# Kernel optimization log

Hardware: AMD Instinct MI355X
Metric: run time of the kernel (lower is better)

Reference implementation:

```python
import jax, jax.numpy as jnp
import numpy as np


def setup_inputs() -> dict:
    key = jax.random.key(0)
    ks = jax.random.split(key, 6)
    B, C, H, W = 8, 128, 64, 64
    return {
        "curr_features": jax.random.normal(ks[0], (B, C, H, W), jnp.float32),
        "w1": jax.random.normal(ks[1], (C, 2 * C), jnp.float32) * 0.05,   # conv1x1 (2C->C)
        "b1": jnp.zeros((C,), jnp.float32),
        "gamma": jnp.ones((C,), jnp.float32),
        "beta": jnp.zeros((C,), jnp.float32),
        "running_mean": jax.random.normal(ks[2], (C,), jnp.float32) * 0.1,
        "running_var": jax.random.uniform(ks[3], (C,), jnp.float32, 0.5, 1.5),
        "w2": jax.random.normal(ks[4], (1, C), jnp.float32) * 0.05,       # conv1x1 (C->1)
        "b2": jnp.zeros((1,), jnp.float32),
    }


def reference(curr_features, w1, b1, gamma, beta, running_mean, running_var, w2, b2):
    B, C, H, W = curr_features.shape
    M = H * W
    BN_EPS = 1e-5
    LEAKY_SLOPE = 0.01  # InPlaceABNSync default activation: leaky_relu(0.01)

    f = curr_features.reshape(B, C, M)                       # [B,C,M]
    scores = jnp.einsum('bcm,bcn->bmn', f, f) * (C ** -0.5)  # [B,M,M]
    p = jax.nn.softmax(scores, axis=-1)
    feats1 = jnp.einsum('bmn,bcn->bcm', p, f)                # [B,C,M]

    x = jnp.concatenate([feats1, f], axis=1).reshape(B, 2 * C, H, W)

    # cls head: conv1x1 -> BN(inference) -> leaky_relu -> (dropout=identity in eval) -> conv1x1
    y = jnp.einsum('oc,bchw->bohw', w1, x) + b1[None, :, None, None]
    scale = gamma / jnp.sqrt(running_var + BN_EPS)
    y = (y - running_mean[None, :, None, None]) * scale[None, :, None, None] + beta[None, :, None, None]
    y = jnp.where(y >= 0, y, LEAKY_SLOPE * y)
    pred = jnp.einsum('oc,bchw->bohw', w2, y) + b2[None, :, None, None]  # [B,1,H,W]
    return pred
```

## Files before the change

### kernel.cpp

```cpp
#include <hip/hip_runtime.h>

#define NB 8
#define NC 128
#define NM 4096
#define FRAG 512

typedef __attribute__((ext_vector_type(8))) short short8;
typedef __attribute__((ext_vector_type(4))) float floatx4;

#define MFMA(a, b, c) __builtin_amdgcn_mfma_f32_16x16x32_bf16(a, b, c, 0, 0, 0)
#define EXP2F(x) __builtin_amdgcn_exp2f(x)

union S8U { short8 v; uint2 u2[2]; };

__device__ __forceinline__ unsigned pack2bf(float a, float b) {
    unsigned ua = __float_as_uint(a);
    unsigned ub = __float_as_uint(b);
    ua += 0x7fffu + ((ua >> 16) & 1u);
    ub += 0x7fffu + ((ub >> 16) & 1u);
    return (ua >> 16) | (ub & 0xffff0000u);
}

__constant__ float SF_C = 0.35712442f;
__constant__ float RS_C = 2.8001530f;


__global__ __launch_bounds__(256) void k_prep_f(
    const float* __restrict__ f, unsigned short* __restrict__ fX)
{
    __shared__ float Ls[128][65];
    const int tid = threadIdx.x;
    const int b   = blockIdx.x & 7;
    const int m0  = (blockIdx.x >> 3) * 64;
    const float* fb = f + (size_t)b * NC * NM;
    #pragma unroll
    for (int k = 0; k < 32; ++k) {
        int idx = tid + k * 256;
        int c = idx >> 6, mm = idx & 63;
        Ls[c][mm] = fb[(size_t)c * NM + m0 + mm];
    }
    __syncthreads();
    const float sf = SF_C;
    const int m  = tid >> 2;
    const int ks = tid & 3;
    const int ch = ks * 32;
    unsigned pk[16];
    #pragma unroll
    for (int i = 0; i < 16; ++i)
        pk[i] = pack2bf(Ls[ch + 2 * i][m] * sf, Ls[ch + 2 * i + 1][m] * sf);
    const int Mg  = m0 + m;
    const int mt  = Mg >> 4;
    const int lmm = Mg & 15;
    unsigned short* dst = fX + ((size_t)b * 256 + mt) * 4 * FRAG + ks * FRAG;
    #pragma unroll
    for (int q = 0; q < 4; ++q)
        *(uint4*)(dst + (q * 16 + lmm) * 8) =
            make_uint4(pk[4 * q], pk[4 * q + 1], pk[4 * q + 2], pk[4 * q + 3]);
}

__global__ __launch_bounds__(256) void k_prep_g(
    const unsigned short* __restrict__ fX, const float* __restrict__ w1,
    unsigned short* __restrict__ gX)
{
    __shared__ unsigned short gt[128][136];
    const int tid = threadIdx.x;
    const int wv  = tid >> 6;
    const int l   = tid & 63;
    const int lm  = l & 15;
    const int lq  = l >> 4;
    const int b    = blockIdx.x & 7;
    const int nblk = blockIdx.x >> 3;

    const float rs = RS_C;

    short8 wf2[2][4];
    #pragma unroll
    for (int j = 0; j < 2; ++j) {
        const int o = (wv * 2 + j) * 16 + lm;
        #pragma unroll
        for (int ks = 0; ks < 4; ++ks) {
            const float* wp = w1 + (size_t)o * (2 * NC) + ks * 32 + lq * 8;
            S8U t;
            t.u2[0] = make_uint2(pack2bf(wp[0] * rs, wp[1] * rs),
                                 pack2bf(wp[2] * rs, wp[3] * rs));
            t.u2[1] = make_uint2(pack2bf(wp[4] * rs, wp[5] * rs),
                                 pack2bf(wp[6] * rs, wp[7] * rs));
            wf2[j][ks] = t.v;
        }
    }

    const unsigned short* fXb = fX + (size_t)b * NM * NC;
    #pragma unroll 2
    for (int nt = 0; nt < 8; ++nt) {
        short8 af[4];
        #pragma unroll
        for (int ks = 0; ks < 4; ++ks)
            af[ks] = *(const short8*)
                (fXb + (size_t)(nblk * 8 + nt) * 4 * FRAG + ks * FRAG + l * 8);
        #pragma unroll
        for (int j = 0; j < 2; ++j) {
            floatx4 D = {0.f, 0.f, 0.f, 0.f};
            #pragma unroll
            for (int ks = 0; ks < 4; ++ks)
                D = MFMA(af[ks], wf2[j][ks], D);
            *(uint2*)&gt[(wv * 2 + j) * 16 + lm][nt * 16 + lq * 4] =
                make_uint2(pack2bf(D[0], D[1]), pack2bf(D[2], D[3]));
        }
    }
    __syncthreads();

    #pragma unroll
    for (int j = 0; j < 2; ++j) {
        const int ot = wv * 2 + j;
        #pragma unroll
        for (int k2 = 0; k2 < 4; ++k2) {
            uint4 v = *(const uint4*)&gt[ot * 16 + lm][k2 * 32 + lq * 8];
            *(uint4*)(gX + (((size_t)b * 32 + nblk) * 8 + ot) * 4 * FRAG
                      + k2 * FRAG + l * 8) = v;
        }
    }
}

__global__ __launch_bounds__(256, 2) void k_attn(
    const unsigned short* __restrict__ fX,
    const unsigned short* __restrict__ gX,
    const float* __restrict__ w1,
    const float* __restrict__ b1v, const float* __restrict__ gammav,
    const float* __restrict__ betav, const float* __restrict__ rmeanv,
    const float* __restrict__ rvarv, const float* __restrict__ w2v,
    const float* __restrict__ b2v, float* __restrict__ out)
{
    __shared__ unsigned short Ps[2][64][136];
    __shared__ float lpart[4][64];
    __shared__ float opart[4][64];

    const int tid = threadIdx.x;
    const int w   = tid >> 6;
    const int l   = tid & 63;
    const int lm  = l & 15;
    const int lq  = l >> 4;
    const int b   = blockIdx.x & 7;
    const int m0  = (blockIdx.x >> 3) * 64;

    const unsigned short* fXb = fX + (size_t)b * NM * NC;
    const unsigned short* gXb = gX + (size_t)b * NC * NM;

    short8 qf[4][4];
    {
        const int qt0 = m0 >> 4;
        #pragma unroll
        for (int mt = 0; mt < 4; ++mt)
            #pragma unroll
            for (int ks = 0; ks < 4; ++ks)
                qf[mt][ks] = *(const short8*)
                    (fXb + (size_t)(qt0 + mt) * 4 * FRAG + ks * FRAG + l * 8);
    }

    const unsigned short* kpA = fXb + (size_t)w * 4 * FRAG + l * 8;
    const unsigned short* kpB = fXb + (size_t)(4 + w) * 4 * FRAG + l * 8;
    const unsigned short* gp0 = gXb + (size_t)(2 * w) * 4 * FRAG + l * 8;
    const unsigned short* gp1 = gXb + (size_t)(2 * w + 1) * 4 * FRAG + l * 8;

    short8 kfA[4], kfB[4], gf0[4], gf1[4];
    #pragma unroll
    for (int ks = 0; ks < 4; ++ks) {
        kfA[ks] = *(const short8*)(kpA + ks * FRAG);
        kfB[ks] = *(const short8*)(kpB + ks * FRAG);
    }
    #pragma unroll
    for (int k2 = 0; k2 < 4; ++k2) {
        gf0[k2] = *(const short8*)(gp0 + k2 * FRAG);
        gf1[k2] = *(const short8*)(gp1 + k2 * FRAG);
    }

    floatx4 u[4][2];
    float lsum[4] = {0.f, 0.f, 0.f, 0.f};
    #pragma unroll
    for (int mt = 0; mt < 4; ++mt) {
        u[mt][0] = (floatx4){0.f, 0.f, 0.f, 0.f};
        u[mt][1] = (floatx4){0.f, 0.f, 0.f, 0.f};
    }

    for (int it = 0; it < 32; ++it) {
        const int buf = it & 1;

        floatx4 svA[4], svB[4];
        #pragma unroll
        for (int mt = 0; mt < 4; ++mt) {
            floatx4 a = {-24.f, -24.f, -24.f, -24.f};
            floatx4 bb = {-24.f, -24.f, -24.f, -24.f};
            #pragma unroll
            for (int ks = 0; ks < 4; ++ks) {
                a  = MFMA(kfA[ks], qf[mt][ks], a);
                bb = MFMA(kfB[ks], qf[mt][ks], bb);
            }
            svA[mt] = a; svB[mt] = bb;
        }
        {
            const int kstep = (it < 31) ? 8 * 4 * FRAG : 0;
            kpA += kstep; kpB += kstep;
            #pragma unroll
            for (int ks = 0; ks < 4; ++ks) {
                kfA[ks] = *(const short8*)(kpA + ks * FRAG);
                kfB[ks] = *(const short8*)(kpB + ks * FRAG);
            }
        }

        #pragma unroll
        for (int mt = 0; mt < 4; ++mt) {
            float pA0 = EXP2F(svA[mt][0]);
            float pA1 = EXP2F(svA[mt][1]);
            float pA2 = EXP2F(svA[mt][2]);
            float pA3 = EXP2F(svA[mt][3]);
            float pB0 = EXP2F(svB[mt][0]);
            float pB1 = EXP2F(svB[mt][1]);
            float pB2 = EXP2F(svB[mt][2]);
            float pB3 = EXP2F(svB[mt][3]);
            lsum[mt] += ((pA0 + pA1) + (pA2 + pA3)) +
                        ((pB0 + pB1) + (pB2 + pB3));
            *(uint2*)&Ps[buf][mt * 16 + lm][w * 16 + lq * 4] =
                make_uint2(pack2bf(pA0, pA1), pack2bf(pA2, pA3));
            *(uint2*)&Ps[buf][mt * 16 + lm][64 + w * 16 + lq * 4] =
                make_uint2(pack2bf(pB0, pB1), pack2bf(pB2, pB3));
        }
        __syncthreads();

        #pragma unroll
        for (int k2 = 0; k2 < 4; ++k2) {
            short8 pf[4];
            #pragma unroll
            for (int mt = 0; mt < 4; ++mt)
                pf[mt] = *(const short8*)&Ps[buf][mt * 16 + lm][k2 * 32 + lq * 8];
            #pragma unroll
            for (int mt = 0; mt < 4; ++mt) {
                u[mt][0] = MFMA(pf[mt], gf0[k2], u[mt][0]);
                u[mt][1] = MFMA(pf[mt], gf1[k2], u[mt][1]);
            }
        }
        {
            const int gstep = (it < 31) ? 8 * 4 * FRAG : 0;
            gp0 += gstep; gp1 += gstep;
            #pragma unroll
            for (int k2 = 0; k2 < 4; ++k2) {
                gf0[k2] = *(const short8*)(gp0 + k2 * FRAG);
                gf1[k2] = *(const short8*)(gp1 + k2 * FRAG);
            }
        }
    }

    #pragma unroll
    for (int mt = 0; mt < 4; ++mt) {
        lsum[mt] += __shfl_xor(lsum[mt], 16);
        lsum[mt] += __shfl_xor(lsum[mt], 32);
    }
    if (lq == 0) {
        #pragma unroll
        for (int mt = 0; mt < 4; ++mt)
            lpart[w][mt * 16 + lm] = lsum[mt];
    }

    floatx4 hacc[4][2];
    {
        const float rs = RS_C;
        #pragma unroll
        for (int j = 0; j < 2; ++j) {
            int o = w * 32 + j * 16 + lm;
            short8 wf[4];
            #pragma unroll
            for (int ks = 0; ks < 4; ++ks) {
                const float* wp = w1 + (size_t)o * (2 * NC) + NC + ks * 32 + lq * 8;
                S8U t;
                t.u2[0] = make_uint2(pack2bf(wp[0] * rs, wp[1] * rs),
                                     pack2bf(wp[2] * rs, wp[3] * rs));
                t.u2[1] = make_uint2(pack2bf(wp[4] * rs, wp[5] * rs),
                                     pack2bf(wp[6] * rs, wp[7] * rs));
                wf[ks] = t.v;
            }
            #pragma unroll
            for (int mt = 0; mt < 4; ++mt) {
                floatx4 a = {0.f, 0.f, 0.f, 0.f};
                #pragma unroll
                for (int ks = 0; ks < 4; ++ks)
                    a = MFMA(qf[mt][ks], wf[ks], a);
                hacc[mt][j] = a;
            }
        }
    }
    __syncthreads();

    float Abn[2], Dbn[2], W2[2];
    #pragma unroll
    for (int j = 0; j < 2; ++j) {
        int o = w * 32 + j * 16 + lm;
        float Ar = gammav[o] * rsqrtf(rvarv[o] + 1e-5f);
        Abn[j] = Ar;
        Dbn[j] = (b1v[o] - rmeanv[o]) * Ar + betav[o];
        W2[j]  = w2v[o];
    }
    float av[16];
    #pragma unroll
    for (int mt = 0; mt < 4; ++mt) {
        float4 L0 = *(const float4*)&lpart[0][mt * 16 + lq * 4];
        float4 L1 = *(const float4*)&lpart[1][mt * 16 + lq * 4];
        float4 L2 = *(const float4*)&lpart[2][mt * 16 + lq * 4];
        float4 L3 = *(const float4*)&lpart[3][mt * 16 + lq * 4];
        float4 Lt;
        Lt.x = (L0.x + L1.x) + (L2.x + L3.x);
        Lt.y = (L0.y + L1.y) + (L2.y + L3.y);
        Lt.z = (L0.z + L1.z) + (L2.z + L3.z);
        Lt.w = (L0.w + L1.w) + (L2.w + L3.w);
        #pragma unroll
        for (int r = 0; r < 4; ++r) {
            float rl = 1.f / ((const float*)&Lt)[r];
            float t0 = Abn[0] * (u[mt][0][r] * rl + hacc[mt][0][r]) + Dbn[0];
            float t1 = Abn[1] * (u[mt][1][r] * rl + hacc[mt][1][r]) + Dbn[1];
            t0 = t0 >= 0.f ? t0 : 0.01f * t0;
            t1 = t1 >= 0.f ? t1 : 0.01f * t1;
            av[mt * 4 + r] = W2[0] * t0 + W2[1] * t1;
        }
    }
    #pragma unroll
    for (int i = 0; i < 16; ++i) {
        av[i] += __shfl_xor(av[i], 1);
        av[i] += __shfl_xor(av[i], 2);
        av[i] += __shfl_xor(av[i], 4);
        av[i] += __shfl_xor(av[i], 8);
    }
    if (lm == 0) {
        #pragma unroll
        for (int mt = 0; mt < 4; ++mt)
            #pragma unroll
            for (int r = 0; r < 4; ++r)
                opart[w][mt * 16 + lq * 4 + r] = av[mt * 4 + r];
    }
    __syncthreads();
    if (tid < 64)
        out[(size_t)b * NM + m0 + tid] =
            b2v[0] + opart[0][tid] + opart[1][tid] + opart[2][tid] + opart[3][tid];
}

extern "C" void kernel_launch(void* const* d_in, const int* in_sizes, int n_in,
                              void* d_out, int out_size, void* d_ws, size_t ws_size,
                              hipStream_t stream) {
    const float* f     = (const float*)d_in[0];
    const float* w1    = (const float*)d_in[1];
    const float* b1    = (const float*)d_in[2];
    const float* gamma = (const float*)d_in[3];
    const float* beta  = (const float*)d_in[4];
    const float* rmean = (const float*)d_in[5];
    const float* rvar  = (const float*)d_in[6];
    const float* w2    = (const float*)d_in[7];
    const float* b2    = (const float*)d_in[8];
    float* out = (float*)d_out;

    unsigned short* fX = (unsigned short*)d_ws;
    unsigned short* gX = fX + (size_t)NB * NM * NC;

    hipLaunchKernelGGL(k_prep_f, dim3(512), dim3(256), 0, stream, f, fX);
    hipLaunchKernelGGL(k_prep_g, dim3(256), dim3(256), 0, stream, fX, w1, gX);
    hipLaunchKernelGGL(k_attn,   dim3(512), dim3(256), 0, stream,
                       fX, gX, w1, b1, gamma, beta, rmean, rvar, w2, b2, out);
}
```

Baseline: 160.1 us.

## Swizzle P tile LDS layout, use hardware bf16 pack, raise MFMA priority

Replaces the padded row-major P staging buffer with a fragment-ordered, XOR-swizzled 16KB-per-buffer layout. Each lane's MFMA operand read becomes a contiguous 16-byte load, and the swizzle is meant to avoid LDS bank conflicts on both writes and reads. The software round-to-nearest bf16 packing is replaced with the v_cvt_pk_bf16_f32 instruction, and s_setprio brackets the MFMA blocks so waves issuing matrix work get priority. The risks are incorrect swizzle index math and possibly different rounding behavior from the hardware conversion.

```diff
diff --git a/kernel.cpp b/kernel.cpp
--- a/kernel.cpp
+++ b/kernel.cpp
@@ -19,6 +19,12 @@
     ua += 0x7fffu + ((ua >> 16) & 1u);
     ub += 0x7fffu + ((ub >> 16) & 1u);
     return (ua >> 16) | (ub & 0xffff0000u);
+}
+
+__device__ __forceinline__ unsigned cvt_pk_bf16(float a, float b) {
+    unsigned r;
+    asm("v_cvt_pk_bf16_f32 %0, %1, %2" : "=v"(r) : "v"(a), "v"(b));
+    return r;
 }
 
 __constant__ float SF_C = 0.35712442f;
@@ -130,7 +136,7 @@
     const float* __restrict__ rvarv, const float* __restrict__ w2v,
     const float* __restrict__ b2v, float* __restrict__ out)
 {
-    __shared__ unsigned short Ps[2][64][136];
+    __shared__ __align__(16) char Ps[2][16384];
     __shared__ float lpart[4][64];
     __shared__ float opart[4][64];
 
@@ -142,6 +148,15 @@
     const int b   = blockIdx.x & 7;
     const int m0  = (blockIdx.x >> 3) * 64;
 
+    const int lq0 = lq & 1;
+    const int lq1 = lq >> 1;
+    const int lm3 = lm >> 3;
+    const unsigned Xsw = (unsigned)(((lq1 << 1) | lm3) << 4);
+    const unsigned wofsA =
+        ((((unsigned)(w >> 1) * 4 * 16) + ((unsigned)(2 * (w & 1) + lq1) * 16)
+          + (unsigned)lm) * 16 + (unsigned)(8 * lq0)) ^ Xsw;
+    const unsigned rofs = ((unsigned)l * 16) ^ ((((unsigned)l >> 3) & 3u) << 4);
+
     const unsigned short* fXb = fX + (size_t)b * NM * NC;
     const unsigned short* gXb = gX + (size_t)b * NC * NM;
 
@@ -183,8 +198,10 @@
 
     for (int it = 0; it < 32; ++it) {
         const int buf = it & 1;
+        char* psb = Ps[buf];
 
         floatx4 svA[4], svB[4];
+        __builtin_amdgcn_s_setprio(1);
         #pragma unroll
         for (int mt = 0; mt < 4; ++mt) {
             floatx4 a = {-24.f, -24.f, -24.f, -24.f};
@@ -196,6 +213,7 @@
             }
             svA[mt] = a; svB[mt] = bb;
         }
+        __builtin_amdgcn_s_setprio(0);
         {
             const int kstep = (it < 31) ? 8 * 4 * FRAG : 0;
             kpA += kstep; kpB += kstep;
@@ -218,10 +236,10 @@
             float pB3 = EXP2F(svB[mt][3]);
             lsum[mt] += ((pA0 + pA1) + (pA2 + pA3)) +
                         ((pB0 + pB1) + (pB2 + pB3));
-            *(uint2*)&Ps[buf][mt * 16 + lm][w * 16 + lq * 4] =
-                make_uint2(pack2bf(pA0, pA1), pack2bf(pA2, pA3));
-            *(uint2*)&Ps[buf][mt * 16 + lm][64 + w * 16 + lq * 4] =
-                make_uint2(pack2bf(pB0, pB1), pack2bf(pB2, pB3));
+            *(uint2*)(psb + mt * 4096 + wofsA) =
+                make_uint2(cvt_pk_bf16(pA0, pA1), cvt_pk_bf16(pA2, pA3));
+            *(uint2*)(psb + mt * 4096 + wofsA + 2048) =
+                make_uint2(cvt_pk_bf16(pB0, pB1), cvt_pk_bf16(pB2, pB3));
         }
         __syncthreads();
 
@@ -230,12 +248,14 @@
             short8 pf[4];
             #pragma unroll
             for (int mt = 0; mt < 4; ++mt)
-                pf[mt] = *(const short8*)&Ps[buf][mt * 16 + lm][k2 * 32 + lq * 8];
+                pf[mt] = *(const short8*)(psb + mt * 4096 + k2 * 1024 + rofs);
+            __builtin_amdgcn_s_setprio(1);
             #pragma unroll
             for (int mt = 0; mt < 4; ++mt) {
                 u[mt][0] = MFMA(pf[mt], gf0[k2], u[mt][0]);
                 u[mt][1] = MFMA(pf[mt], gf1[k2], u[mt][1]);
             }
+            __builtin_amdgcn_s_setprio(0);
         }
         {
             const int gstep = (it < 31) ? 8 * 4 * FRAG : 0;
```

New measurement: 156.9 us. -2.0%, faster.
